# Kernel optimization log

Measured on AMD Instinct MI355X. Metric: run time of the kernel, lower is better.

Reference implementation:

```python
import jax, jax.numpy as jnp
import numpy as np

B, C, O = 16384, 128, 128


def setup_inputs() -> dict:
    key = jax.random.key(0)
    k1, k2, k3 = jax.random.split(key, 3)
    x = jax.random.normal(k1, (B, C, 3, 3), dtype=jnp.float32)
    # 9 stacked Conv2d(C, O, 3x3) weights/biases, position p = 3*r + c (row-major)
    W = jax.random.normal(k2, (9, O, C, 3, 3), dtype=jnp.float32) * 0.05
    b = jax.random.normal(k3, (9, O), dtype=jnp.float32) * 0.05
    return {"x": x, "W": W, "b": b}


def reference(x, W, b):
    Bn = x.shape[0]
    xr = x.reshape(Bn, C, 3, 3)
    # F.interpolate(scale_factor=3, mode='nearest'): each pixel replicated 3x3
    ins = jnp.repeat(jnp.repeat(xr, 3, axis=2), 3, axis=3)  # (B, C, 9, 9)
    # patch for output position (r, c) is ins[:, :, 2+r:5+r, 2+c:5+c]
    patches = jnp.stack(
        [ins[:, :, 2 + r:5 + r, 2 + c:5 + c] for r in range(3) for c in range(3)],
        axis=0,
    )  # (9, B, C, 3, 3)
    # each conv reduces its 3x3xC patch to one pixel per out-channel
    out = jnp.einsum('pbcij,pocij->bpo', patches, W) + b[None]  # (B, 9, O)
    out = out.transpose(0, 2, 1).reshape(Bn, O, 3, 3)  # row-major (r, c)
    return out
```

## Files before the change

### kernel.cpp

```cpp
#include <hip/hip_runtime.h>
#include <hip/hip_bf16.h>

typedef __bf16 bf16_t;
typedef __attribute__((ext_vector_type(8))) __bf16 bf16x8;
typedef __attribute__((ext_vector_type(4))) float f32x4;

#define KDIM 1152
#define NDIM 1152
#define BM 128
#define BN 288
#define BK 32
#define NIT 36
#define NTILES 4
#define AF_STEP 16384
#define B_STEP 18432
#define B_TILE (36 * B_STEP)

__device__ __forceinline__ void gload_lds16(const void* g, void* l) {
    __builtin_amdgcn_global_load_lds(
        (const __attribute__((address_space(1))) void*)g,
        (__attribute__((address_space(3))) void*)l, 16, 0, 0);
}

__global__ void build_wb(const float* __restrict__ W,
                         const float* __restrict__ bvec,
                         bf16_t* __restrict__ Bm,
                         float* __restrict__ bias)
{
    const int t = blockIdx.x * blockDim.x + threadIdx.x;
    if (t < NDIM) {
        const int o = t / 9, p = t - o * 9;
        bias[t] = bvec[p * 128 + o];
    }
    const int c = t & 127;
    const int o = (t >> 7) & 127;
    const int p = t >> 14;
    if (p >= 9) return;
    const int r = p / 3, cc = p - r * 3;
    float eff[3][3] = {{0.f,0.f,0.f},{0.f,0.f,0.f},{0.f,0.f,0.f}};
    const float* w = W + (size_t)((p * 128 + o) * 128 + c) * 9;
    #pragma unroll
    for (int i = 0; i < 3; ++i) {
        const int a = (2 + r + i) / 3;
        #pragma unroll
        for (int j = 0; j < 3; ++j) {
            const int bb = (2 + cc + j) / 3;
            eff[a][bb] += w[i * 3 + j];
        }
    }
    const int n = o * 9 + p;
    const int tile = n / BN;
    const int nin = n - tile * BN;
    #pragma unroll
    for (int a = 0; a < 3; ++a)
        #pragma unroll
        for (int bb = 0; bb < 3; ++bb) {
            const int k = c * 9 + a * 3 + bb;
            const size_t idx = (size_t)tile * (B_TILE / 2)
                             + (k >> 5) * (B_STEP / 2)
                             + (nin >> 4) * 512 + ((k >> 3) & 3) * 128
                             + (nin & 15) * 8 + (k & 7);
            Bm[idx] = (bf16_t)eff[a][bb];
        }
}

__launch_bounds__(256, 2)
__global__ void ind_gemm(const float* __restrict__ X,
                         const bf16_t* __restrict__ Bm,
                         const float* __restrict__ bias,
                         float* __restrict__ out)
{
    __shared__ char Af[2][AF_STEP];
    __shared__ char Bs[2][B_STEP];
    __shared__ char Scrap[1024];

    const int tid = threadIdx.x;
    const int lane = tid & 63;
    const int wid = tid >> 6;
    const int wm = wid >> 1;
    const int wn = wid & 1;

    const int bid = blockIdx.x;
    const int swz = (bid & 7) * 64 + (bid >> 3);
    const int mt = swz >> 2;
    const int nt = swz & 3;
    const int m0 = mt * BM;

    const int row0 = tid >> 3;
    const int kb0 = (tid & 7) ^ (row0 & 7);
    const char* asrc = (const char*)(X + (size_t)(m0 + row0) * KDIM + kb0 * 4);

    const int abase = (wm * 64 + (lane & 15)) * 128;
    const int g2 = (lane >> 4) * 2;
    const int x0 = ((g2)     ^ (lane & 7)) * 16;
    const int x1 = ((g2 + 1) ^ (lane & 7)) * 16;

    const int fr = (lane >> 4) * 256 + (lane & 15) * 16;
    const char* bpanel = (const char*)Bm + (size_t)nt * B_TILE;

    f32x4 acc[4][9];
    #pragma unroll
    for (int i = 0; i < 4; ++i)
        #pragma unroll
        for (int j = 0; j < 9; ++j)
            acc[i][j] = (f32x4){0.f, 0.f, 0.f, 0.f};

    f32x4 alo[4], ahi[4];
    bf16x8 bfr[9];

    #define GLD(T, BUF) do {                                                \
        const char* sa_ = asrc + (size_t)(T) * 128;                         \
        _Pragma("unroll")                                                   \
        for (int r_ = 0; r_ < 4; ++r_)                                      \
            gload_lds16(sa_ + (size_t)r_ * 147456,                          \
                        &Af[BUF][tid * 16 + r_ * 4096]);                    \
        const char* sb_ = bpanel + (size_t)(T) * B_STEP;                    \
        _Pragma("unroll")                                                   \
        for (int r_ = 0; r_ < 4; ++r_) {                                    \
            const int u_ = (tid + r_ * 256) * 16;                           \
            gload_lds16(sb_ + u_, &Bs[BUF][u_]);                            \
        }                                                                   \
        if (tid < 128) gload_lds16(sb_ + (1024 + tid) * 16,                 \
                                   &Bs[BUF][(1024 + tid) * 16]);            \
        else           gload_lds16(bpanel + tid * 16, Scrap);               \
    } while (0)

    #define RD(CUR) do {                                                    \
        _Pragma("unroll")                                                   \
        for (int mi_ = 0; mi_ < 4; ++mi_) {                                 \
            alo[mi_] = *(const f32x4*)(&Af[CUR][abase + mi_ * 2048 + x0]);  \
            ahi[mi_] = *(const f32x4*)(&Af[CUR][abase + mi_ * 2048 + x1]);  \
        }                                                                   \
        _Pragma("unroll")                                                   \
        for (int j_ = 0; j_ < 9; ++j_)                                      \
            bfr[j_] = *(const bf16x8*)(&Bs[CUR][(wn * 9 + j_) * 1024 + fr]); \
        asm volatile("s_waitcnt lgkmcnt(0)" ::: "memory");                  \
        __builtin_amdgcn_sched_barrier(0);                                  \
        __builtin_amdgcn_s_barrier();                                       \
    } while (0)

    #define MFMA36() do {                                                   \
        __builtin_amdgcn_s_setprio(1);                                      \
        _Pragma("unroll")                                                   \
        for (int mi_ = 0; mi_ < 4; ++mi_) {                                 \
            bf16x8 a_;                                                      \
            _Pragma("unroll")                                               \
            for (int e_ = 0; e_ < 4; ++e_) {                                \
                a_[e_]     = (__bf16)alo[mi_][e_];                          \
                a_[4 + e_] = (__bf16)ahi[mi_][e_];                          \
            }                                                               \
            _Pragma("unroll")                                               \
            for (int j_ = 0; j_ < 9; ++j_)                                  \
                acc[mi_][j_] = __builtin_amdgcn_mfma_f32_16x16x32_bf16(     \
                    a_, bfr[j_], acc[mi_][j_], 0, 0, 0);                    \
        }                                                                   \
        __builtin_amdgcn_s_setprio(0);                                      \
    } while (0)

    #define WAITV(N) do {                                                   \
        asm volatile("s_waitcnt vmcnt(" #N ")" ::: "memory");               \
        __builtin_amdgcn_sched_barrier(0);                                  \
    } while (0)

    GLD(0, 0);
    GLD(1, 1);
    WAITV(9);
    __builtin_amdgcn_s_barrier();

    #pragma unroll 1
    for (int t2 = 0; t2 < 17; ++t2) {
        const int t = 2 * t2;
        RD(0);
        GLD(t + 2, 0);
        MFMA36();
        WAITV(9);
        __builtin_amdgcn_s_barrier();
        RD(1);
        GLD(t + 3, 1);
        MFMA36();
        WAITV(9);
        __builtin_amdgcn_s_barrier();
    }
    RD(0);
    MFMA36();
    WAITV(0);
    __builtin_amdgcn_s_barrier();
    RD(1);
    MFMA36();

    #undef GLD
    #undef RD
    #undef MFMA36
    #undef WAITV

    const int orow = (lane >> 4) * 4;
    const int ocol = lane & 15;
    const int gn0 = nt * BN + wn * 144 + ocol;
    #pragma unroll
    for (int ni = 0; ni < 9; ++ni) {
        const float bv = bias[gn0 + ni * 16];
        #pragma unroll
        for (int mi = 0; mi < 4; ++mi) {
            float* po = out + (size_t)(m0 + wm * 64 + mi * 16 + orow) * NDIM
                            + gn0 + ni * 16;
            #pragma unroll
            for (int r = 0; r < 4; ++r)
                po[(size_t)r * NDIM] = acc[mi][ni][r] + bv;
        }
    }
}

extern "C" void kernel_launch(void* const* d_in, const int* in_sizes, int n_in,
                              void* d_out, int out_size, void* d_ws, size_t ws_size,
                              hipStream_t stream)
{
    const float* x  = (const float*)d_in[0];
    const float* W  = (const float*)d_in[1];
    const float* bv = (const float*)d_in[2];
    float* out = (float*)d_out;

    bf16_t* Bm   = (bf16_t*)d_ws;
    float*  bias = (float*)((char*)d_ws + (size_t)KDIM * NDIM * sizeof(bf16_t));

    build_wb<<<576, 256, 0, stream>>>(W, bv, Bm, bias);
    ind_gemm<<<512, 256, 0, stream>>>(x, Bm, bias, out);
}
```

Before: 75.42 us.

## Load A via registers, convert to bf16 once, store bf16 tile in LDS

Replaces the direct global-to-LDS copy of fp32 A tiles with register loads that are converted to bf16 by the loading thread and written to LDS in the MFMA fragment layout. This halves the A tile size in LDS and removes per-wave redundant fp32-to-bf16 conversion inside the MFMA loop, since each A element was previously converted by both N-warps. The pipeline is restructured so the register loads run one stage ahead of the LDS stores. The cost is extra VGPRs, explicit LDS stores, and a more intricate wait/barrier schedule that can stall on global latency.

```diff
diff --git a/kernel.cpp b/kernel.cpp
--- a/kernel.cpp
+++ b/kernel.cpp
@@ -12,7 +12,7 @@
 #define BK 32
 #define NIT 36
 #define NTILES 4
-#define AF_STEP 16384
+#define AB_STEP 8192
 #define B_STEP 18432
 #define B_TILE (36 * B_STEP)
 
@@ -70,7 +70,7 @@
                          const float* __restrict__ bias,
                          float* __restrict__ out)
 {
-    __shared__ char Af[2][AF_STEP];
+    __shared__ char Af[2][AB_STEP];
     __shared__ char Bs[2][B_STEP];
     __shared__ char Scrap[1024];
 
@@ -86,15 +86,10 @@
     const int nt = swz & 3;
     const int m0 = mt * BM;
 
-    const int row0 = tid >> 3;
-    const int kb0 = (tid & 7) ^ (row0 & 7);
-    const char* asrc = (const char*)(X + (size_t)(m0 + row0) * KDIM + kb0 * 4);
-
-    const int abase = (wm * 64 + (lane & 15)) * 128;
-    const int g2 = (lane >> 4) * 2;
-    const int x0 = ((g2)     ^ (lane & 7)) * 16;
-    const int x1 = ((g2 + 1) ^ (lane & 7)) * 16;
-
+    const int arow = (tid >> 5) * 16 + 2 * (tid & 7);
+    const char* a_src  = (const char*)(X + (size_t)(m0 + arow) * KDIM
+                                         + ((tid >> 3) & 3) * 8);
+    const char* a_src2 = a_src + (size_t)KDIM * 4;
     const int fr = (lane >> 4) * 256 + (lane & 15) * 16;
     const char* bpanel = (const char*)Bm + (size_t)nt * B_TILE;
 
@@ -105,15 +100,36 @@
         for (int j = 0; j < 9; ++j)
             acc[i][j] = (f32x4){0.f, 0.f, 0.f, 0.f};
 
-    f32x4 alo[4], ahi[4];
-    bf16x8 bfr[9];
-
-    #define GLD(T, BUF) do {                                                \
-        const char* sa_ = asrc + (size_t)(T) * 128;                         \
-        _Pragma("unroll")                                                   \
-        for (int r_ = 0; r_ < 4; ++r_)                                      \
-            gload_lds16(sa_ + (size_t)r_ * 147456,                          \
-                        &Af[BUF][tid * 16 + r_ * 4096]);                    \
+    f32x4 ra[4];
+    bf16x8 af[4], bfr[9];
+
+    #define LOADA(T) do {                                                   \
+        const char* p0_ = a_src  + (size_t)(T) * 128;                       \
+        const char* p1_ = a_src2 + (size_t)(T) * 128;                       \
+        asm volatile("global_load_dwordx4 %0, %2, off\n\t"                  \
+                     "global_load_dwordx4 %1, %2, off offset:16"            \
+                     : "=&v"(ra[0]), "=&v"(ra[1])                           \
+                     : "v"(p0_) : "memory");                                \
+        asm volatile("global_load_dwordx4 %0, %2, off\n\t"                  \
+                     "global_load_dwordx4 %1, %2, off offset:16"            \
+                     : "=&v"(ra[2]), "=&v"(ra[3])                           \
+                     : "v"(p1_) : "memory");                                \
+    } while (0)
+
+    #define CVTW(BUF) do {                                                  \
+        bf16x8 w0_, w1_;                                                    \
+        _Pragma("unroll")                                                   \
+        for (int e_ = 0; e_ < 4; ++e_) {                                    \
+            w0_[e_]     = (__bf16)ra[0][e_];                                \
+            w0_[4 + e_] = (__bf16)ra[1][e_];                                \
+            w1_[e_]     = (__bf16)ra[2][e_];                                \
+            w1_[4 + e_] = (__bf16)ra[3][e_];                                \
+        }                                                                   \
+        *(bf16x8*)(&Af[BUF][tid * 32])      = w0_;                          \
+        *(bf16x8*)(&Af[BUF][tid * 32 + 16]) = w1_;                          \
+    } while (0)
+
+    #define GLDB(T, BUF) do {                                               \
         const char* sb_ = bpanel + (size_t)(T) * B_STEP;                    \
         _Pragma("unroll")                                                   \
         for (int r_ = 0; r_ < 4; ++r_) {                                    \
@@ -127,10 +143,8 @@
 
     #define RD(CUR) do {                                                    \
         _Pragma("unroll")                                                   \
-        for (int mi_ = 0; mi_ < 4; ++mi_) {                                 \
-            alo[mi_] = *(const f32x4*)(&Af[CUR][abase + mi_ * 2048 + x0]);  \
-            ahi[mi_] = *(const f32x4*)(&Af[CUR][abase + mi_ * 2048 + x1]);  \
-        }                                                                   \
+        for (int mi_ = 0; mi_ < 4; ++mi_)                                   \
+            af[mi_] = *(const bf16x8*)(&Af[CUR][(wm * 4 + mi_) * 1024 + fr]); \
         _Pragma("unroll")                                                   \
         for (int j_ = 0; j_ < 9; ++j_)                                      \
             bfr[j_] = *(const bf16x8*)(&Bs[CUR][(wn * 9 + j_) * 1024 + fr]); \
@@ -142,18 +156,11 @@
     #define MFMA36() do {                                                   \
         __builtin_amdgcn_s_setprio(1);                                      \
         _Pragma("unroll")                                                   \
-        for (int mi_ = 0; mi_ < 4; ++mi_) {                                 \
-            bf16x8 a_;                                                      \
-            _Pragma("unroll")                                               \
-            for (int e_ = 0; e_ < 4; ++e_) {                                \
-                a_[e_]     = (__bf16)alo[mi_][e_];                          \
-                a_[4 + e_] = (__bf16)ahi[mi_][e_];                          \
-            }                                                               \
+        for (int mi_ = 0; mi_ < 4; ++mi_)                                   \
             _Pragma("unroll")                                               \
             for (int j_ = 0; j_ < 9; ++j_)                                  \
                 acc[mi_][j_] = __builtin_amdgcn_mfma_f32_16x16x32_bf16(     \
-                    a_, bfr[j_], acc[mi_][j_], 0, 0, 0);                    \
-        }                                                                   \
+                    af[mi_], bfr[j_], acc[mi_][j_], 0, 0, 0);               \
         __builtin_amdgcn_s_setprio(0);                                      \
     } while (0)
 
@@ -162,33 +169,61 @@
         __builtin_amdgcn_sched_barrier(0);                                  \
     } while (0)
 
-    GLD(0, 0);
-    GLD(1, 1);
+    LOADA(0);
+    WAITV(0);
+    CVTW(0);
+    LOADA(1);
+    GLDB(0, 0);
+    GLDB(1, 1);
+    WAITV(10);
+    CVTW(1);
+    LOADA(2);
     WAITV(9);
+    asm volatile("s_waitcnt lgkmcnt(0)" ::: "memory");
+    __builtin_amdgcn_sched_barrier(0);
     __builtin_amdgcn_s_barrier();
 
     #pragma unroll 1
-    for (int t2 = 0; t2 < 17; ++t2) {
+    for (int t2 = 0; t2 < 16; ++t2) {
         const int t = 2 * t2;
         RD(0);
-        GLD(t + 2, 0);
+        GLDB(t + 2, 0);
+        WAITV(5);
+        CVTW(0);
+        LOADA(t + 3);
         MFMA36();
-        WAITV(9);
         __builtin_amdgcn_s_barrier();
         RD(1);
-        GLD(t + 3, 1);
+        GLDB(t + 3, 1);
+        WAITV(5);
+        CVTW(1);
+        LOADA(t + 4);
         MFMA36();
-        WAITV(9);
         __builtin_amdgcn_s_barrier();
     }
     RD(0);
-    MFMA36();
+    GLDB(34, 0);
+    WAITV(5);
+    CVTW(0);
+    LOADA(35);
+    MFMA36();
+    __builtin_amdgcn_s_barrier();
+    RD(1);
+    GLDB(35, 1);
+    WAITV(5);
+    CVTW(1);
+    MFMA36();
+    __builtin_amdgcn_s_barrier();
+    RD(0);
     WAITV(0);
+    MFMA36();
     __builtin_amdgcn_s_barrier();
     RD(1);
     MFMA36();
 
-    #undef GLD
+    #undef LOADA
+    #undef CVTW
+    #undef GLDB
     #undef RD
     #undef MFMA36
     #undef WAITV
```

After: 84.04 us. 11.4% more time.
